# Kernel tuning notes

Measured on AMD Instinct MI355X. Metric: run time of the kernel, lower is better.

The kernel has to match this reference:

```python
import jax, jax.numpy as jnp
import numpy as np


def setup_inputs() -> dict:
    key = jax.random.key(0)
    ks = jax.random.split(key, 8)
    B, C, N = 4, 256, 4096
    C4 = C // 4
    x = jax.random.normal(ks[0], (B, C, N), dtype=jnp.float32)
    # conv1x1 weights == channel-mixing matrices [out_ch, in_ch]
    Wq = jax.random.normal(ks[1], (C4, C), dtype=jnp.float32) * (1.0 / np.sqrt(C))
    bq = jax.random.normal(ks[2], (C4,), dtype=jnp.float32) * 0.02
    Wk = jax.random.normal(ks[3], (C4, C), dtype=jnp.float32) * (1.0 / np.sqrt(C))
    bk = jax.random.normal(ks[4], (C4,), dtype=jnp.float32) * 0.02
    Wv = jax.random.normal(ks[5], (C, C), dtype=jnp.float32) * (1.0 / np.sqrt(C))
    bv = jax.random.normal(ks[6], (C,), dtype=jnp.float32) * 0.02
    # nn.Parameter(torch.zeros(1)) -> but use nonzero so grads flow through attn path
    gamma = jax.random.normal(ks[7], (1,), dtype=jnp.float32) * 0.1
    return {"x": x, "Wq": Wq, "bq": bq, "Wk": Wk, "bk": bk,
            "Wv": Wv, "bv": bv, "gamma": gamma}


def reference(x, Wq, bq, Wk, bk, Wv, bv, gamma):
    # x: [B, C, N]; conv1x1 == matmul over channel dim
    q = jnp.einsum('oc,bcn->bon', Wq, x) + bq[None, :, None]   # [B, C/4, N]
    k = jnp.einsum('oc,bcn->bon', Wk, x) + bk[None, :, None]   # [B, C/4, N]
    v = jnp.einsum('oc,bcn->bon', Wv, x) + bv[None, :, None]   # [B, C,   N]
    # energy[b, i, j] = <q[:, i], k[:, j]>  (unscaled)
    energy = jnp.einsum('bdi,bdj->bij', q, k)                  # [B, N, N]
    attn = jax.nn.softmax(energy, axis=-1)                     # softmax over j
    # out[b, c, i] = sum_j v[b, c, j] * attn[b, i, j]
    out = jnp.einsum('bcj,bij->bci', v, attn)                  # [B, C, N]
    return gamma[0] * out + x
```

## Files before the change

### kernel.cpp

```cpp
#include <hip/hip_runtime.h>

#define NPTS 4096
#define CDIM 256
#define C4DIM 64

typedef __bf16 bf16x8 __attribute__((ext_vector_type(8)));
typedef float  f32x4  __attribute__((ext_vector_type(4)));

__device__ __forceinline__ void async_cp16(const void* g, void* l) {
    __builtin_amdgcn_global_load_lds(
        (const __attribute__((address_space(1))) void*)g,
        (__attribute__((address_space(3))) void*)l, 16, 0, 0);
}

__global__ __launch_bounds__(256) void wprep_kernel(
    const float* __restrict__ Wq, const float* __restrict__ Wk,
    const float* __restrict__ Wv, __bf16* __restrict__ wsz)
{
    int idx = blockIdx.x * 256 + threadIdx.x;
    int row = idx >> 6;
    int l   = idx & 63;
    const float* src;
    if (row < 64)       src = Wq + (size_t)row * CDIM;
    else if (row < 128) src = Wk + (size_t)(row - 64) * CDIM;
    else                src = Wv + (size_t)(row - 128) * CDIM;
    float4 f = *(const float4*)&src[l * 4];
    int g  = l >> 1;
    int gp = g ^ (row & 7);
    union { __bf16 h[4]; uint2 u; } pk;
    pk.h[0] = (__bf16)f.x; pk.h[1] = (__bf16)f.y;
    pk.h[2] = (__bf16)f.z; pk.h[3] = (__bf16)f.w;
    *(uint2*)&wsz[(size_t)row * CDIM + gp * 8 + (l & 1) * 4] = pk.u;
}

__global__ __launch_bounds__(256, 1) void proj_kernel(
    const float* __restrict__ x,
    const float* __restrict__ bq, const float* __restrict__ bk,
    const float* __restrict__ bv, const __bf16* __restrict__ wsz,
    __bf16* __restrict__ qT, __bf16* __restrict__ kT, __bf16* __restrict__ vo)
{
    __shared__ __align__(16) unsigned char sm[83968];
    auto Xs = (float (*)[65])sm;
    auto OT = (float (*)[68])(sm + 66560);

    const int t    = threadIdx.x;
    const int w    = t >> 6;
    const int lane = t & 63;
    const int quad = lane >> 4;
    const int l16  = lane & 15;

    const int n0 = blockIdx.x * 64;
    const int b  = blockIdx.y;

    #pragma unroll
    for (int s = 0; s < 16; s++) {
        int lin = t + 256 * s;
        int c = lin >> 4, n4 = (lin & 15) * 4;
        *(float4*)&Xs[c][n4] =
            *(const float4*)&x[((size_t)b * CDIM + c) * NPTS + n0 + n4];
    }
    __syncthreads();

    bf16x8 af[8];
    #pragma unroll
    for (int kc = 0; kc < 8; kc++) {
        union { __bf16 h8[8]; bf16x8 v; } pk;
        #pragma unroll
        for (int u = 0; u < 8; u++)
            pk.h8[u] = (__bf16)Xs[kc * 32 + quad * 8 + u][16 * w + l16];
        af[kc] = pk.v;
    }
    __syncthreads();

    const int lhalf = lane >> 5;
    const int rlow  = (2 * w + lhalf) & 7;
    const int slane = ((lane & 31) ^ rlow) * 8;

    #pragma unroll
    for (int s = 0; s < 8; s++)
        async_cp16(wsz + (size_t)(8 * s + 2 * w + lhalf) * CDIM + slane,
                   sm + (s * 4 + w) * 1024);

    f32x4 acc[6][4];
    #pragma unroll
    for (int ot = 0; ot < 6; ot++)
        #pragma unroll
        for (int tc = 0; tc < 4; tc++) acc[ot][tc] = (f32x4)(0.f);

    #pragma unroll
    for (int ot = 0; ot < 6; ot++) {
        __syncthreads();
        if (ot < 5) {
            #pragma unroll
            for (int s = 0; s < 8; s++)
                async_cp16(wsz + (size_t)((ot + 1) * 64 + 8 * s + 2 * w + lhalf) * CDIM + slane,
                           sm + ((ot + 1) & 1) * 32768 + (s * 4 + w) * 1024);
        }
        const unsigned char* Wp = sm + (ot & 1) * 32768;
        #pragma unroll
        for (int kc = 0; kc < 8; kc++) {
            bf16x8 bw[4];
            #pragma unroll
            for (int tc = 0; tc < 4; tc++)
                bw[tc] = *(const bf16x8*)(Wp + (16 * tc + l16) * 512
                                             + (((kc * 4 + quad) ^ (l16 & 7)) << 4));
            #pragma unroll
            for (int tc = 0; tc < 4; tc++)
                acc[ot][tc] = __builtin_amdgcn_mfma_f32_16x16x32_bf16(
                    af[kc], bw[tc], acc[ot][tc], 0, 0, 0);
        }
    }

    #pragma unroll
    for (int ot = 0; ot < 2; ot++) {
        __syncthreads();
        const float* bias = ot ? bk : bq;
        #pragma unroll
        for (int tc = 0; tc < 4; tc++) {
            float bs = bias[16 * tc + l16];
            #pragma unroll
            for (int r4 = 0; r4 < 4; r4++)
                OT[16 * w + 4 * quad + r4][16 * tc + l16] = acc[ot][tc][r4] + bs;
        }
        __syncthreads();
        __bf16* outp = (ot == 0 ? qT : kT) + (size_t)b * NPTS * C4DIM;
        int n = t >> 2, op = (t & 3) * 16;
        union { __bf16 h[16]; uint4 u[2]; } pk;
        #pragma unroll
        for (int u2 = 0; u2 < 16; u2++) pk.h[u2] = (__bf16)OT[n][op + u2];
        *(uint4*)&outp[(size_t)(n0 + n) * C4DIM + op]     = pk.u[0];
        *(uint4*)&outp[(size_t)(n0 + n) * C4DIM + op + 8] = pk.u[1];
    }
    #pragma unroll
    for (int ot = 2; ot < 6; ot++) {
        __syncthreads();
        #pragma unroll
        for (int tc = 0; tc < 4; tc++) {
            float bs = bv[(ot - 2) * 64 + 16 * tc + l16];
            f32x4 v4 = acc[ot][tc];
            v4[0] += bs; v4[1] += bs; v4[2] += bs; v4[3] += bs;
            *(f32x4*)&OT[16 * tc + l16][16 * w + 4 * quad] = v4;
        }
        __syncthreads();
        int cl = t >> 2, np = (t & 3) * 16;
        int ch = (ot - 2) * 64 + cl;
        union { __bf16 h[16]; uint4 u[2]; } pk;
        #pragma unroll
        for (int u2 = 0; u2 < 16; u2++) pk.h[u2] = (__bf16)OT[cl][np + u2];
        __bf16* outp = vo + ((size_t)b * CDIM + ch) * NPTS + n0 + np;
        *(uint4*)&outp[0] = pk.u[0];
        *(uint4*)&outp[8] = pk.u[1];
    }
}

__global__ __launch_bounds__(256, 2) void attn_kernel(
    const __bf16* __restrict__ qT, const __bf16* __restrict__ kT,
    const __bf16* __restrict__ vin, const float* __restrict__ xin,
    const float* __restrict__ gptr, float* __restrict__ out)
{
    __shared__ __align__(16) unsigned char sm[58368];
    unsigned char* Kb = sm;
    unsigned char* Vb = sm + 16384;
    auto Ps  = (__bf16 (*)[72])(sm + 49152);
    auto OTa = (float (*)[68])(sm);
    float* Lp = (float*)(sm + 34816);

    const int t    = threadIdx.x;
    const int w    = t >> 6;
    const int lane = t & 63;
    const int quad = lane >> 4;
    const int l16  = lane & 15;
    const int r    = w >> 1;
    const int jh   = w & 1;

    const int b  = blockIdx.z;
    const int i0 = blockIdx.x * 64;
    const int c0 = blockIdx.y * 128;

    const __bf16* qb = qT  + (size_t)b * NPTS * C4DIM;
    const __bf16* kb = kT  + (size_t)b * NPTS * C4DIM;
    const __bf16* vb = vin + (size_t)b * CDIM * NPTS;

    const int swz = (lane & 7) ^ ((lane >> 3) & 7);
    int koff[2], voff[4];
    #pragma unroll
    for (int s = 0; s < 2; s++) {
        int row = (2 * w + s) * 8 + (lane >> 3);
        koff[s] = row * 128 + swz * 16;
    }
    #pragma unroll
    for (int s = 0; s < 4; s++) {
        int row = (4 * w + s) * 8 + (lane >> 3);
        voff[s] = (c0 + row) * (NPTS * 2) + swz * 16;
    }

    bf16x8 aq[2][2];
    #pragma unroll
    for (int rt = 0; rt < 2; rt++)
        #pragma unroll
        for (int kc = 0; kc < 2; kc++)
            aq[rt][kc] = *(const bf16x8*)&qb[(size_t)(i0 + 32 * r + 16 * rt + l16) * C4DIM
                                             + kc * 32 + quad * 8];

    bf16x8 vone;
    #pragma unroll
    for (int u = 0; u < 8; u++) vone[u] = (__bf16)1.0f;

    f32x4 O[2][8], lacc[2];
    #pragma unroll
    for (int rt = 0; rt < 2; rt++) {
        lacc[rt] = (f32x4)(0.f);
        #pragma unroll
        for (int tc = 0; tc < 8; tc++) O[rt][tc] = (f32x4)(0.f);
    }

    {
        const char* kbase = (const char*)kb;
        const char* vbase = (const char*)vb;
        #pragma unroll
        for (int s = 0; s < 2; s++) async_cp16(kbase + koff[s], Kb + (2 * w + s) * 1024);
        #pragma unroll
        for (int s = 0; s < 4; s++) async_cp16(vbase + voff[s], Vb + (4 * w + s) * 1024);
    }

    int p = 0;
    for (int j0 = 0; j0 < NPTS; j0 += 64, p ^= 1) {
        __syncthreads();

        if (j0 + 64 < NPTS) {
            const char* kbase = (const char*)kb + (size_t)(j0 + 64) * (C4DIM * 2);
            const char* vbase = (const char*)vb + (size_t)(j0 + 64) * 2;
            unsigned char* Kd = Kb + (p ^ 1) * 8192;
            unsigned char* Vd = Vb + (p ^ 1) * 16384;
            #pragma unroll
            for (int s = 0; s < 2; s++) async_cp16(kbase + koff[s], Kd + (2 * w + s) * 1024);
            #pragma unroll
            for (int s = 0; s < 4; s++) async_cp16(vbase + voff[s], Vd + (4 * w + s) * 1024);
        }

        const unsigned char* K = Kb + p * 8192;
        const unsigned char* V = Vb + p * 16384;

        f32x4 S[2][2];
        #pragma unroll
        for (int rt = 0; rt < 2; rt++)
            #pragma unroll
            for (int ct = 0; ct < 2; ct++) S[rt][ct] = (f32x4)(0.f);
        #pragma unroll
        for (int kc = 0; kc < 2; kc++) {
            bf16x8 bk2[2];
            #pragma unroll
            for (int ct = 0; ct < 2; ct++) {
                int row = 32 * jh + 16 * ct + l16;
                int slot = (kc * 4 + quad) ^ (l16 & 7);
                bk2[ct] = *(const bf16x8*)(K + row * 128 + slot * 16);
            }
            #pragma unroll
            for (int rt = 0; rt < 2; rt++)
                #pragma unroll
                for (int ct = 0; ct < 2; ct++)
                    S[rt][ct] = __builtin_amdgcn_mfma_f32_16x16x32_bf16(
                        aq[rt][kc], bk2[ct], S[rt][ct], 0, 0, 0);
        }

        #pragma unroll
        for (int rt = 0; rt < 2; rt++)
            #pragma unroll
            for (int ct = 0; ct < 2; ct++)
                #pragma unroll
                for (int r4 = 0; r4 < 4; r4++)
                    Ps[32 * r + 16 * rt + 4 * quad + r4][32 * jh + 16 * ct + l16] =
                        (__bf16)__expf(S[rt][ct][r4] - 32.0f);

        bf16x8 ap[2];
        #pragma unroll
        for (int rt = 0; rt < 2; rt++)
            ap[rt] = *(const bf16x8*)((const char*)&Ps[32 * r + 16 * rt + l16][0]
                                      + jh * 64 + quad * 16);
        #pragma unroll
        for (int tc = 0; tc < 8; tc++) {
            int row = 16 * tc + l16;
            int slot = (jh * 4 + quad) ^ (l16 & 7);
            bf16x8 bv2 = *(const bf16x8*)(V + row * 128 + slot * 16);
            #pragma unroll
            for (int rt = 0; rt < 2; rt++)
                O[rt][tc] = __builtin_amdgcn_mfma_f32_16x16x32_bf16(
                    ap[rt], bv2, O[rt][tc], 0, 0, 0);
        }
        #pragma unroll
        for (int rt = 0; rt < 2; rt++)
            lacc[rt] = __builtin_amdgcn_mfma_f32_16x16x32_bf16(ap[rt], vone, lacc[rt], 0, 0, 0);
    }

    __syncthreads();
    const float g = gptr[0];

    if (jh == 1) {
        float* dst = (float*)(sm + (size_t)(r * 64 + lane) * 272);
        #pragma unroll
        for (int rt = 0; rt < 2; rt++)
            #pragma unroll
            for (int tc = 0; tc < 8; tc++)
                *(f32x4*)(dst + (rt * 8 + tc) * 4) = O[rt][tc];
        if (l16 == 0) {
            #pragma unroll
            for (int rt = 0; rt < 2; rt++)
                #pragma unroll
                for (int r4 = 0; r4 < 4; r4++)
                    Lp[32 * r + 16 * rt + 4 * quad + r4] = lacc[rt][r4];
        }
    }
    __syncthreads();

    float inv[2][4];
    if (jh == 0) {
        const float* src = (const float*)(sm + (size_t)(r * 64 + lane) * 272);
        #pragma unroll
        for (int rt = 0; rt < 2; rt++)
            #pragma unroll
            for (int tc = 0; tc < 8; tc++)
                O[rt][tc] += *(const f32x4*)(src + (rt * 8 + tc) * 4);
        #pragma unroll
        for (int rt = 0; rt < 2; rt++)
            #pragma unroll
            for (int r4 = 0; r4 < 4; r4++) {
                float ls = lacc[rt][r4] + Lp[32 * r + 16 * rt + 4 * quad + r4];
                inv[rt][r4] = g / ls;
            }
    }
    __syncthreads();

    if (jh == 0) {
        #pragma unroll
        for (int rt = 0; rt < 2; rt++)
            #pragma unroll
            for (int tc = 0; tc < 8; tc++) {
                int c = 16 * tc + l16;
                float4 f;
                f.x = O[rt][tc][0] * inv[rt][0];
                f.y = O[rt][tc][1] * inv[rt][1];
                f.z = O[rt][tc][2] * inv[rt][2];
                f.w = O[rt][tc][3] * inv[rt][3];
                *(float4*)&OTa[c][32 * r + 16 * rt + 4 * quad] = f;
            }
    }
    __syncthreads();

    const float* xb = xin + (size_t)b * CDIM * NPTS;
    float*       ob = out + (size_t)b * CDIM * NPTS;
    #pragma unroll
    for (int s = 0; s < 8; s++) {
        int lin = t + 256 * s;
        int c = lin >> 4, col = (lin & 15) * 4;
        size_t gi = (size_t)(c0 + c) * NPTS + i0 + col;
        float4 ov = *(const float4*)&OTa[c][col];
        float4 xv = *(const float4*)&xb[gi];
        float4 rr;
        rr.x = ov.x + xv.x; rr.y = ov.y + xv.y;
        rr.z = ov.z + xv.z; rr.w = ov.w + xv.w;
        *(float4*)&ob[gi] = rr;
    }
}

extern "C" void kernel_launch(void* const* d_in, const int* in_sizes, int n_in,
                              void* d_out, int out_size, void* d_ws, size_t ws_size,
                              hipStream_t stream) {
    const float* x     = (const float*)d_in[0];
    const float* Wq    = (const float*)d_in[1];
    const float* bq    = (const float*)d_in[2];
    const float* Wk    = (const float*)d_in[3];
    const float* bk    = (const float*)d_in[4];
    const float* Wv    = (const float*)d_in[5];
    const float* bv    = (const float*)d_in[6];
    const float* gamma = (const float*)d_in[7];

    const int B = 4;
    __bf16* qT  = (__bf16*)d_ws;
    __bf16* kT  = qT + (size_t)B * NPTS * C4DIM;
    __bf16* v   = kT + (size_t)B * NPTS * C4DIM;
    __bf16* wsz = v  + (size_t)B * CDIM * NPTS;

    wprep_kernel<<<96, 256, 0, stream>>>(Wq, Wk, Wv, wsz);

    proj_kernel<<<dim3(NPTS/64, B), 256, 0, stream>>>(
        x, bq, bk, bv, wsz, qT, kT, v);

    attn_kernel<<<dim3(NPTS/64, CDIM/128, B), 256, 0, stream>>>(
        qT, kT, v, x, gamma, (float*)d_out);
}
```

Measured before the change: 168.5 us.

## Split projection across two blocks per tile and read weights directly from global

The projection kernel now launches twice as many blocks, each computing three of the six 64-row output tiles. This should raise occupancy and parallelism. Staging through LDS is removed: x is read straight from global with strided scalar loads, and the weights are read as unswizzled rows from global instead of being prefetched asynchronously into swizzled shared memory. The weight prep drops the XOR swizzle to match. In exchange, x is loaded twice, and the global loads are less coalesced with no double-buffered prefetch.

```diff
diff --git a/kernel.cpp b/kernel.cpp
--- a/kernel.cpp
+++ b/kernel.cpp
@@ -19,29 +19,25 @@
 {
     int idx = blockIdx.x * 256 + threadIdx.x;
     int row = idx >> 6;
-    int l   = idx & 63;
+    int l4  = idx & 63;
     const float* src;
     if (row < 64)       src = Wq + (size_t)row * CDIM;
     else if (row < 128) src = Wk + (size_t)(row - 64) * CDIM;
     else                src = Wv + (size_t)(row - 128) * CDIM;
-    float4 f = *(const float4*)&src[l * 4];
-    int g  = l >> 1;
-    int gp = g ^ (row & 7);
+    float4 f = *(const float4*)&src[l4 * 4];
     union { __bf16 h[4]; uint2 u; } pk;
     pk.h[0] = (__bf16)f.x; pk.h[1] = (__bf16)f.y;
     pk.h[2] = (__bf16)f.z; pk.h[3] = (__bf16)f.w;
-    *(uint2*)&wsz[(size_t)row * CDIM + gp * 8 + (l & 1) * 4] = pk.u;
-}
-
-__global__ __launch_bounds__(256, 1) void proj_kernel(
+    *(uint2*)&wsz[(size_t)row * CDIM + l4 * 4] = pk.u;
+}
+
+__global__ __launch_bounds__(256) void proj_kernel(
     const float* __restrict__ x,
     const float* __restrict__ bq, const float* __restrict__ bk,
     const float* __restrict__ bv, const __bf16* __restrict__ wsz,
     __bf16* __restrict__ qT, __bf16* __restrict__ kT, __bf16* __restrict__ vo)
 {
-    __shared__ __align__(16) unsigned char sm[83968];
-    auto Xs = (float (*)[65])sm;
-    auto OT = (float (*)[68])(sm + 66560);
+    __shared__ float OT[64][68];
 
     const int t    = threadIdx.x;
     const int w    = t >> 6;
@@ -49,107 +45,81 @@
     const int quad = lane >> 4;
     const int l16  = lane & 15;
 
-    const int n0 = blockIdx.x * 64;
-    const int b  = blockIdx.y;
-
-    #pragma unroll
-    for (int s = 0; s < 16; s++) {
-        int lin = t + 256 * s;
-        int c = lin >> 4, n4 = (lin & 15) * 4;
-        *(float4*)&Xs[c][n4] =
-            *(const float4*)&x[((size_t)b * CDIM + c) * NPTS + n0 + n4];
-    }
-    __syncthreads();
+    const int n0   = blockIdx.x * 64;
+    const int half = blockIdx.y;
+    const int b    = blockIdx.z;
 
     bf16x8 af[8];
+    const float* xb = x + (size_t)b * CDIM * NPTS + n0 + 16 * w + l16;
     #pragma unroll
     for (int kc = 0; kc < 8; kc++) {
         union { __bf16 h8[8]; bf16x8 v; } pk;
         #pragma unroll
         for (int u = 0; u < 8; u++)
-            pk.h8[u] = (__bf16)Xs[kc * 32 + quad * 8 + u][16 * w + l16];
+            pk.h8[u] = (__bf16)xb[(size_t)(kc * 32 + quad * 8 + u) * NPTS];
         af[kc] = pk.v;
     }
-    __syncthreads();
-
-    const int lhalf = lane >> 5;
-    const int rlow  = (2 * w + lhalf) & 7;
-    const int slane = ((lane & 31) ^ rlow) * 8;
-
-    #pragma unroll
-    for (int s = 0; s < 8; s++)
-        async_cp16(wsz + (size_t)(8 * s + 2 * w + lhalf) * CDIM + slane,
-                   sm + (s * 4 + w) * 1024);
-
-    f32x4 acc[6][4];
-    #pragma unroll
-    for (int ot = 0; ot < 6; ot++)
-        #pragma unroll
-        for (int tc = 0; tc < 4; tc++) acc[ot][tc] = (f32x4)(0.f);
-
-    #pragma unroll
-    for (int ot = 0; ot < 6; ot++) {
-        __syncthreads();
-        if (ot < 5) {
-            #pragma unroll
-            for (int s = 0; s < 8; s++)
-                async_cp16(wsz + (size_t)((ot + 1) * 64 + 8 * s + 2 * w + lhalf) * CDIM + slane,
-                           sm + ((ot + 1) & 1) * 32768 + (s * 4 + w) * 1024);
-        }
-        const unsigned char* Wp = sm + (ot & 1) * 32768;
+
+    #pragma unroll
+    for (int ti = 0; ti < 3; ti++) {
+        const int ot = half * 3 + ti;
+        const __bf16* Wt = wsz + (size_t)ot * 64 * CDIM;
+
+        f32x4 acc[4];
+        #pragma unroll
+        for (int tc = 0; tc < 4; tc++) acc[tc] = (f32x4)(0.f);
+
         #pragma unroll
         for (int kc = 0; kc < 8; kc++) {
             bf16x8 bw[4];
             #pragma unroll
             for (int tc = 0; tc < 4; tc++)
-                bw[tc] = *(const bf16x8*)(Wp + (16 * tc + l16) * 512
-                                             + (((kc * 4 + quad) ^ (l16 & 7)) << 4));
+                bw[tc] = *(const bf16x8*)&Wt[(size_t)(16 * tc + l16) * CDIM
+                                             + kc * 32 + quad * 8];
             #pragma unroll
             for (int tc = 0; tc < 4; tc++)
-                acc[ot][tc] = __builtin_amdgcn_mfma_f32_16x16x32_bf16(
-                    af[kc], bw[tc], acc[ot][tc], 0, 0, 0);
-        }
-    }
-
-    #pragma unroll
-    for (int ot = 0; ot < 2; ot++) {
-        __syncthreads();
-        const float* bias = ot ? bk : bq;
-        #pragma unroll
-        for (int tc = 0; tc < 4; tc++) {
-            float bs = bias[16 * tc + l16];
-            #pragma unroll
-            for (int r4 = 0; r4 < 4; r4++)
-                OT[16 * w + 4 * quad + r4][16 * tc + l16] = acc[ot][tc][r4] + bs;
-        }
-        __syncthreads();
-        __bf16* outp = (ot == 0 ? qT : kT) + (size_t)b * NPTS * C4DIM;
-        int n = t >> 2, op = (t & 3) * 16;
-        union { __bf16 h[16]; uint4 u[2]; } pk;
-        #pragma unroll
-        for (int u2 = 0; u2 < 16; u2++) pk.h[u2] = (__bf16)OT[n][op + u2];
-        *(uint4*)&outp[(size_t)(n0 + n) * C4DIM + op]     = pk.u[0];
-        *(uint4*)&outp[(size_t)(n0 + n) * C4DIM + op + 8] = pk.u[1];
-    }
-    #pragma unroll
-    for (int ot = 2; ot < 6; ot++) {
-        __syncthreads();
-        #pragma unroll
-        for (int tc = 0; tc < 4; tc++) {
-            float bs = bv[(ot - 2) * 64 + 16 * tc + l16];
-            f32x4 v4 = acc[ot][tc];
-            v4[0] += bs; v4[1] += bs; v4[2] += bs; v4[3] += bs;
-            *(f32x4*)&OT[16 * tc + l16][16 * w + 4 * quad] = v4;
-        }
-        __syncthreads();
-        int cl = t >> 2, np = (t & 3) * 16;
-        int ch = (ot - 2) * 64 + cl;
-        union { __bf16 h[16]; uint4 u[2]; } pk;
-        #pragma unroll
-        for (int u2 = 0; u2 < 16; u2++) pk.h[u2] = (__bf16)OT[cl][np + u2];
-        __bf16* outp = vo + ((size_t)b * CDIM + ch) * NPTS + n0 + np;
-        *(uint4*)&outp[0] = pk.u[0];
-        *(uint4*)&outp[8] = pk.u[1];
+                acc[tc] = __builtin_amdgcn_mfma_f32_16x16x32_bf16(
+                    af[kc], bw[tc], acc[tc], 0, 0, 0);
+        }
+
+        if (ot < 2) {
+            const float* bias = ot ? bk : bq;
+            __syncthreads();
+            #pragma unroll
+            for (int tc = 0; tc < 4; tc++) {
+                float bs = bias[16 * tc + l16];
+                #pragma unroll
+                for (int r4 = 0; r4 < 4; r4++)
+                    OT[16 * w + 4 * quad + r4][16 * tc + l16] = acc[tc][r4] + bs;
+            }
+            __syncthreads();
+            __bf16* outp = (ot == 0 ? qT : kT) + (size_t)b * NPTS * C4DIM;
+            int n = t >> 2, op = (t & 3) * 16;
+            union { __bf16 h[16]; uint4 u[2]; } pk;
+            #pragma unroll
+            for (int u2 = 0; u2 < 16; u2++) pk.h[u2] = (__bf16)OT[n][op + u2];
+            *(uint4*)&outp[(size_t)(n0 + n) * C4DIM + op]     = pk.u[0];
+            *(uint4*)&outp[(size_t)(n0 + n) * C4DIM + op + 8] = pk.u[1];
+        } else {
+            const int vs = ot - 2;
+            __syncthreads();
+            #pragma unroll
+            for (int tc = 0; tc < 4; tc++) {
+                float bs = bv[vs * 64 + 16 * tc + l16];
+                f32x4 v4 = acc[tc];
+                v4[0] += bs; v4[1] += bs; v4[2] += bs; v4[3] += bs;
+                *(f32x4*)&OT[16 * tc + l16][16 * w + 4 * quad] = v4;
+            }
+            __syncthreads();
+            int cl = t >> 2, np = (t & 3) * 16;
+            int ch = vs * 64 + cl;
+            union { __bf16 h[16]; uint4 u[2]; } pk;
+            #pragma unroll
+            for (int u2 = 0; u2 < 16; u2++) pk.h[u2] = (__bf16)OT[cl][np + u2];
+            __bf16* outp = vo + ((size_t)b * CDIM + ch) * NPTS + n0 + np;
+            *(uint4*)&outp[0] = pk.u[0];
+            *(uint4*)&outp[8] = pk.u[1];
+        }
     }
 }
 
@@ -382,7 +352,7 @@
 
     wprep_kernel<<<96, 256, 0, stream>>>(Wq, Wk, Wv, wsz);
 
-    proj_kernel<<<dim3(NPTS/64, B), 256, 0, stream>>>(
+    proj_kernel<<<dim3(NPTS/64, 2, B), 256, 0, stream>>>(
         x, bq, bk, bv, wsz, qT, kT, v);
 
     attn_kernel<<<dim3(NPTS/64, CDIM/128, B), 256, 0, stream>>>(
```

Result: slower. 184.6 us (+9.5%).
